# Performance work log

Measured on AMD Instinct MI355X. Metric: run time of the kernel, lower is better.

The kernel has to match this reference:

```python
import jax, jax.numpy as jnp
import numpy as np

B_, J_, D_, E_, N_, K_ = 32, 1024, 192, 384, 16, 3


def _dwconv(x, w, b):
    # x: (B,J,E), w: (E,1,K) depthwise, b: (E,)
    xc = jnp.transpose(x, (0, 2, 1))  # (B,E,J)
    pad = w.shape[2] // 2
    y = jax.lax.conv_general_dilated(
        xc, w, window_strides=(1,), padding=[(pad, pad)],
        feature_group_count=w.shape[0], dimension_numbers=('NCH', 'OIH', 'NCH'))
    return jnp.transpose(y + b[None, :, None], (0, 2, 1))  # (B,J,E)


def _scan_dir(x, cw, cb, WB, bB, WC, bC, WD, bD, A, Wi, bi, Wr, br):
    # One directional selective-SSM pass. x: (B,J,E); A: (N,) negative diag.
    xc = _dwconv(x, cw, cb)                       # (B,J,E)
    Bt = xc @ WB + bB                             # (B,J,N)
    Ct = xc @ WC + bC                             # (B,J,N)
    Dt = jax.nn.softplus(xc @ WD + bD)            # Delta, (B,J,N)
    A_bar = jnp.exp(Dt * A)                       # ZOH discretization
    B_bar = (A_bar - 1.0) / (A + 1e-6) * Bt
    u = xc @ Wi + bi                              # in_to_state, (B,J,N)
    Bu = B_bar * u

    def step(h, ab_bu):
        ab, bu = ab_bu
        h = ab * h + bu
        return h, h

    h0 = jnp.zeros((x.shape[0], A.shape[0]), x.dtype)
    _, hs = jax.lax.scan(step, h0, (jnp.swapaxes(A_bar, 0, 1), jnp.swapaxes(Bu, 0, 1)))
    hs = jnp.swapaxes(hs, 0, 1)                   # (B,J,N)
    return (hs * Ct) @ Wr + br                    # readout, (B,J,E)


def setup_inputs() -> dict:
    key = jax.random.key(0)
    ks = iter(jax.random.split(key, 40))

    def nrm(shape, scale=0.02):
        return jax.random.normal(next(ks), shape, jnp.float32) * scale

    inp = {
        'tokens': jax.random.normal(next(ks), (B_, J_, D_), jnp.float32),
        'norm_g': jnp.ones((D_,), jnp.float32),
        'norm_b': jnp.zeros((D_,), jnp.float32),
        'Wx': nrm((D_, E_)), 'bx': jnp.zeros((E_,), jnp.float32),
        'Wz': nrm((D_, E_)), 'bz': jnp.zeros((E_,), jnp.float32),
        'convf_w': nrm((E_, 1, K_), 0.1), 'convf_b': jnp.zeros((E_,), jnp.float32),
        'convb_w': nrm((E_, 1, K_), 0.1), 'convb_b': jnp.zeros((E_,), jnp.float32),
        'WBf': nrm((E_, N_)), 'bBf': jnp.zeros((N_,), jnp.float32),
        'WCf': nrm((E_, N_)), 'bCf': jnp.zeros((N_,), jnp.float32),
        'WDf': nrm((E_, N_)), 'bDf': jnp.zeros((N_,), jnp.float32),
        'WBb': nrm((E_, N_)), 'bBb': jnp.zeros((N_,), jnp.float32),
        'WCb': nrm((E_, N_)), 'bCb': jnp.zeros((N_,), jnp.float32),
        'WDb': nrm((E_, N_)), 'bDb': jnp.zeros((N_,), jnp.float32),
        'A_log': nrm((N_,), 0.5),
        'Wi': nrm((E_, N_)), 'bi': jnp.zeros((N_,), jnp.float32),
        'Wr': nrm((N_, E_)), 'br': jnp.zeros((E_,), jnp.float32),
        'Wo': nrm((E_, D_)), 'bo': jnp.zeros((D_,), jnp.float32),
    }
    return inp


def reference(tokens, norm_g, norm_b, Wx, bx, Wz, bz, convf_w, convf_b,
              convb_w, convb_b, WBf, bBf, WCf, bCf, WDf, bDf, WBb, bBb,
              WCb, bCb, WDb, bDb, A_log, Wi, bi, Wr, br, Wo, bo):
    # LayerNorm (biased variance, eps=1e-5, like torch)
    mu = jnp.mean(tokens, axis=-1, keepdims=True)
    var = jnp.mean(jnp.square(tokens - mu), axis=-1, keepdims=True)
    t = (tokens - mu) / jnp.sqrt(var + 1e-5) * norm_g + norm_b

    x = t @ Wx + bx
    z = t @ Wz + bz
    gate = jax.nn.sigmoid(jax.nn.silu(z))

    # A computed under no_grad in torch -> stop_gradient here
    A = jax.lax.stop_gradient(-jax.nn.softplus(A_log))

    y_f = _scan_dir(x, convf_w, convf_b, WBf, bBf, WCf, bCf, WDf, bDf, A, Wi, bi, Wr, br)
    y_b = jnp.flip(_scan_dir(jnp.flip(x, 1), convb_w, convb_b, WBb, bBb, WCb, bCb,
                             WDb, bDb, A, Wi, bi, Wr, br), 1)
    y = (y_f + y_b) * gate
    return tokens + y @ Wo + bo
```

## Files before the change

### kernel.cpp

```cpp
#include <hip/hip_runtime.h>
#include <math.h>


typedef __attribute__((ext_vector_type(8))) short short8;
typedef __attribute__((ext_vector_type(4))) float f32x4;

__device__ __forceinline__ unsigned short f2bf(float f){
  union { float f; unsigned u; } v; v.f = f;
  unsigned r = v.u + 0x7FFFu + ((v.u >> 16) & 1u);
  return (unsigned short)(r >> 16);
}
__device__ __forceinline__ float bf2f(unsigned short s){
  union { unsigned u; float f; } v; v.u = ((unsigned)s) << 16;
  return v.f;
}
__device__ __forceinline__ float softplusf(float x){
  return (x > 20.f) ? x : log1pf(expf(x));
}
__device__ __forceinline__ float softplus_fast(float x){
  return (x > 20.f) ? x : __logf(1.f + __expf(x));
}
__device__ __forceinline__ float sigf_fast(float x){
  return __builtin_amdgcn_rcpf(1.f + __expf(-x));
}

__global__ __launch_bounds__(256) void prep_kernel(
    const float* __restrict__ Wx, const float* __restrict__ Wz,
    const float* __restrict__ WBf, const float* __restrict__ WCf,
    const float* __restrict__ WDf, const float* __restrict__ WBb,
    const float* __restrict__ WCb, const float* __restrict__ WDb,
    const float* __restrict__ Wi, const float* __restrict__ Wr,
    const float* __restrict__ Wo,
    const float* __restrict__ bBf, const float* __restrict__ bCf,
    const float* __restrict__ bDf, const float* __restrict__ bBb,
    const float* __restrict__ bCb, const float* __restrict__ bDb,
    const float* __restrict__ bi,
    unsigned short* __restrict__ Wxz_t, unsigned short* __restrict__ W4f_t,
    unsigned short* __restrict__ W4b_t, unsigned short* __restrict__ Wrt2,
    unsigned short* __restrict__ Wot, float* __restrict__ b4f,
    float* __restrict__ b4b)
{
  int idx = blockIdx.x * 256 + threadIdx.x;
  if (idx < 147456){ int n = idx / 192, k = idx % 192;
    Wxz_t[idx] = f2bf(n < 384 ? Wx[k*384 + n] : Wz[k*384 + n - 384]); return; }
  idx -= 147456;
  if (idx < 24576){ int n = idx / 384, k = idx % 384;
    const float* W = (n<16)?WBf:(n<32)?WCf:(n<48)?WDf:Wi;
    W4f_t[idx] = f2bf(W[k*16 + (n&15)]); return; }
  idx -= 24576;
  if (idx < 24576){ int n = idx / 384, k = idx % 384;
    const float* W = (n<16)?WBb:(n<32)?WCb:(n<48)?WDb:Wi;
    W4b_t[idx] = f2bf(W[k*16 + (n&15)]); return; }
  idx -= 24576;
  if (idx < 12288){ int n = idx / 32, k = idx % 32;
    Wrt2[idx] = f2bf(Wr[(k&15)*384 + n]); return; }
  idx -= 12288;
  if (idx < 73728){ int n = idx / 384, k = idx % 384;
    Wot[idx] = f2bf(Wo[k*192 + n]); return; }
  idx -= 73728;
  if (idx < 64){
    const float* bsel = (idx<16)?bBf:(idx<32)?bCf:(idx<48)?bDf:bi;
    b4f[idx] = bsel[idx & 15]; return; }
  idx -= 64;
  if (idx < 64){
    const float* bsel = (idx<16)?bBb:(idx<32)?bCb:(idx<48)?bDb:bi;
    b4b[idx] = bsel[idx & 15]; return; }
}

__global__ __launch_bounds__(256) void ln_kernel(
    const float* __restrict__ tokens, const float* __restrict__ g,
    const float* __restrict__ nb, unsigned short* __restrict__ t_bf)
{
  __shared__ unsigned short s[32 * 200];
  const int t = threadIdx.x;
  const int row0 = blockIdx.x * 32;
  {
    const int r = t >> 3, l8 = t & 7;
    const float* tr = tokens + (long)(row0 + r) * 192;
    float v[24], sm = 0.f, sq = 0.f;
#pragma unroll
    for (int i = 0; i < 24; i++){ float x = tr[l8 + 8*i]; v[i] = x; sm += x; sq += x*x; }
#pragma unroll
    for (int m = 1; m < 8; m <<= 1){ sm += __shfl_xor(sm, m); sq += __shfl_xor(sq, m); }
    const float mu = sm * (1.f/192.f);
    const float rstd = rsqrtf(sq * (1.f/192.f) - mu*mu + 1e-5f);
#pragma unroll
    for (int i = 0; i < 24; i++){
      const int d = l8 + 8*i;
      s[r*200 + d] = f2bf((v[i] - mu)*rstd*g[d] + nb[d]);
    }
  }
  __syncthreads();
  {
#pragma unroll
    for (int i = 0; i < 3; i++){
      const int item = i*256 + t;
      const int row = item / 24, c8 = item % 24;
      *(short8*)&t_bf[(long)(row0 + row)*192 + c8*8] =
          *(const short8*)&s[row*200 + c8*8];
    }
  }
}

__global__ __launch_bounds__(256) void xz_gemm(
    const unsigned short* __restrict__ t_bf,
    const unsigned short* __restrict__ Wxz_t,
    const float* __restrict__ bx, const float* __restrict__ bz,
    unsigned short* __restrict__ x_bf, unsigned short* __restrict__ gate_bf)
{
  __shared__ unsigned short tl[64 * 200];
  const int t = threadIdx.x;
  const int ct = blockIdx.x % 6;
  const int rt = blockIdx.x / 6;
  const int row0 = rt * 64;

  {
#pragma unroll
    for (int i = 0; i < 6; i++){
      const int item = i*256 + t;
      const int row = item / 24, c8 = item % 24;
      *(short8*)&tl[row*200 + c8*8] =
          *(const short8*)&t_bf[(long)(row0 + row)*192 + c8*8];
    }
  }
  __syncthreads();

  const int lane = t & 63, w = t >> 6;
  const int l15 = lane & 15, q = lane >> 4;
  const int C0 = ct*128 + w*32;

  f32x4 acc[4][2];
#pragma unroll
  for (int m = 0; m < 4; m++)
#pragma unroll
    for (int nf = 0; nf < 2; nf++) acc[m][nf] = (f32x4){0.f,0.f,0.f,0.f};

  const unsigned short* wb = Wxz_t + (long)(C0 + l15)*192 + q*8;
#pragma unroll
  for (int ks = 0; ks < 6; ks++){
    const int k0 = ks * 32;
    short8 a0 = *(const short8*)&tl[(     l15)*200 + k0 + q*8];
    short8 a1 = *(const short8*)&tl[(16 + l15)*200 + k0 + q*8];
    short8 a2 = *(const short8*)&tl[(32 + l15)*200 + k0 + q*8];
    short8 a3 = *(const short8*)&tl[(48 + l15)*200 + k0 + q*8];
#pragma unroll
    for (int nf = 0; nf < 2; nf++){
      short8 bw = *(const short8*)&wb[nf*16*192 + k0];
      acc[0][nf] = __builtin_amdgcn_mfma_f32_16x16x32_bf16(a0, bw, acc[0][nf], 0, 0, 0);
      acc[1][nf] = __builtin_amdgcn_mfma_f32_16x16x32_bf16(a1, bw, acc[1][nf], 0, 0, 0);
      acc[2][nf] = __builtin_amdgcn_mfma_f32_16x16x32_bf16(a2, bw, acc[2][nf], 0, 0, 0);
      acc[3][nf] = __builtin_amdgcn_mfma_f32_16x16x32_bf16(a3, bw, acc[3][nf], 0, 0, 0);
    }
  }
  __syncthreads();

  unsigned short* stg = tl;
  const int isgate = (ct >= 3);
#pragma unroll
  for (int nf = 0; nf < 2; nf++){
    const int c = C0 + nf*16 + l15;
    const float bv = isgate ? bz[c - 384] : bx[c];
#pragma unroll
    for (int m = 0; m < 4; m++){
#pragma unroll
      for (int r = 0; r < 4; r++){
        float val = acc[m][nf][r] + bv;
        if (isgate){ const float si = val * sigf_fast(val); val = sigf_fast(si); }
        stg[(m*16 + q*4 + r)*136 + (w*32 + nf*16 + l15)] = f2bf(val);
      }
    }
  }
  __syncthreads();

  {
    unsigned short* outp = isgate ? gate_bf : x_bf;
    const int cb = isgate ? (ct*128 - 384) : (ct*128);
#pragma unroll
    for (int i = 0; i < 4; i++){
      const int item = i*256 + t;
      const int row = item / 16, c8 = item % 16;
      *(short8*)&outp[(long)(row0 + row)*384 + cb + c8*8] =
          *(const short8*)&stg[row*136 + c8*8];
    }
  }
}

__global__ __launch_bounds__(256) void proj_mfma(
    const unsigned short* __restrict__ x_bf,
    const float* __restrict__ cwf, const float* __restrict__ cbf,
    const float* __restrict__ cwb, const float* __restrict__ cbb,
    const unsigned short* __restrict__ W4f, const unsigned short* __restrict__ W4b,
    const float* __restrict__ b4f, const float* __restrict__ b4b,
    const float* __restrict__ A_log,
    float* __restrict__ Af, float* __restrict__ Buf, float* __restrict__ Ctf,
    float* __restrict__ Ab, float* __restrict__ Bub, float* __restrict__ Ctb)
{
  __shared__ unsigned short xc[32 * 392];
  float* pj = (float*)xc;
  const int t = threadIdx.x;
  const int dir = blockIdx.x >> 10;
  const int bid = blockIdx.x & 1023;
  const int b  = bid >> 5;
  const int j0 = (bid & 31) * 32;
  const float* cw = dir ? cwb : cwf;
  const float* cb = dir ? cbb : cbf;
  const unsigned short* W4 = dir ? W4b : W4f;
  const float* b4 = dir ? b4b : b4f;
  float* Aout = dir ? Ab  : Af;
  float* Bout = dir ? Bub : Buf;
  float* Cout = dir ? Ctb : Ctf;

  {
    const long xrow = (long)b * 1024 * 384;
#pragma unroll
    for (int i = 0; i < 6; i++){
      const int idx = i*256 + t;
      const int r = idx / 48;
      const int e0 = (idx - r*48) * 8;
      const int jp = j0 + r;
      short8 xm = (short8){0,0,0,0,0,0,0,0};
      short8 xp = (short8){0,0,0,0,0,0,0,0};
      if (jp >= 1){
        const int js = dir ? 1024 - jp : jp - 1;
        xm = *(const short8*)&x_bf[xrow + (long)js*384 + e0];
      }
      short8 x0;
      {
        const int js = dir ? 1023 - jp : jp;
        x0 = *(const short8*)&x_bf[xrow + (long)js*384 + e0];
      }
      if (jp <= 1022){
        const int js = dir ? 1022 - jp : jp + 1;
        xp = *(const short8*)&x_bf[xrow + (long)js*384 + e0];
      }
      float wv[24], cbv[8];
#pragma unroll
      for (int v = 0; v < 6; v++)
        *(float4*)&wv[v*4] = *(const float4*)&cw[e0*3 + v*4];
#pragma unroll
      for (int v = 0; v < 2; v++)
        *(float4*)&cbv[v*4] = *(const float4*)&cb[e0 + v*4];
      short8 o;
#pragma unroll
      for (int m = 0; m < 8; m++){
        const float acc = fmaf(wv[3*m],   bf2f((unsigned short)xm[m]),
                          fmaf(wv[3*m+1], bf2f((unsigned short)x0[m]),
                          fmaf(wv[3*m+2], bf2f((unsigned short)xp[m]), cbv[m])));
        o[m] = (short)f2bf(acc);
      }
      *(short8*)&xc[r*392 + e0] = o;
    }
  }
  __syncthreads();

  const int lane = t & 63, w = t >> 6;
  const int l15 = lane & 15, q = lane >> 4;
  const int rt = w & 1, ng = w >> 1;
  f32x4 acc[2];
#pragma unroll
  for (int nf = 0; nf < 2; nf++) acc[nf] = (f32x4){0.f,0.f,0.f,0.f};
  const unsigned short* wb = W4 + (long)(ng*32 + l15)*384 + q*8;
#pragma unroll
  for (int ks = 0; ks < 12; ks++){
    const int k0 = ks * 32;
    short8 a = *(const short8*)&xc[(rt*16 + l15)*392 + k0 + q*8];
#pragma unroll
    for (int nf = 0; nf < 2; nf++){
      short8 bw = *(const short8*)&wb[nf*16*384 + k0];
      acc[nf] = __builtin_amdgcn_mfma_f32_16x16x32_bf16(a, bw, acc[nf], 0, 0, 0);
    }
  }
  __syncthreads();

  {
#pragma unroll
    for (int nf = 0; nf < 2; nf++){
      const int col = ng*32 + nf*16 + l15;
#pragma unroll
      for (int r = 0; r < 4; r++)
        pj[col*34 + rt*16 + q*4 + r] = acc[nf][r];
    }
  }
  __syncthreads();

  {
#pragma unroll
    for (int i = 0; i < 2; i++){
      const int idx = i*256 + t;
      const int n = idx >> 5, j = idx & 31;
      const float Bt  = pj[(     n)*34 + j] + b4[n];
      const float Ctv = pj[(16 + n)*34 + j] + b4[16 + n];
      const float dt  = softplus_fast(pj[(32 + n)*34 + j] + b4[32 + n]);
      const float u   = pj[(48 + n)*34 + j] + b4[48 + n];
      const float Av  = -softplusf(A_log[n]);
      const float ab  = __expf(dt * Av);
      const float bu  = (ab - 1.f) * __builtin_amdgcn_rcpf(Av + 1e-6f) * Bt * u;
      const int jp = j0 + j;
      const long base = ((long)b*16 + n) * 1024;
      Aout[base + jp] = ab;
      Bout[base + jp] = bu;
      Cout[base + (dir ? 1023 - jp : jp)] = Ctv;
    }
  }
}

__global__ __launch_bounds__(256) void scan2_kernel(
    const float* __restrict__ Af, const float* __restrict__ Buf, float* __restrict__ hsf,
    const float* __restrict__ Ab, const float* __restrict__ Bub, float* __restrict__ hsb)
{
  __shared__ float sA[256], sB[256];
  const int sel = blockIdx.x >> 9;
  const long base = (long)(blockIdx.x & 511) * 1024;
  const float* Abar = sel ? Ab  : Af;
  const float* Bu   = sel ? Bub : Buf;
  float* hs         = sel ? hsb : hsf;
  const int t = threadIdx.x;
  const float4 a4 = *reinterpret_cast<const float4*>(&Abar[base + t*4]);
  const float4 b4 = *reinterpret_cast<const float4*>(&Bu[base + t*4]);
  float A = a4.x, Bc = b4.x;
  Bc = fmaf(a4.y, Bc, b4.y); A *= a4.y;
  Bc = fmaf(a4.z, Bc, b4.z); A *= a4.z;
  Bc = fmaf(a4.w, Bc, b4.w); A *= a4.w;
  sA[t] = A; sB[t] = Bc;
  __syncthreads();
  for (int off = 1; off < 256; off <<= 1){
    const float cA = sA[t], cB = sB[t];
    float pA = 1.f, pB = 0.f;
    if (t >= off){ pA = sA[t - off]; pB = sB[t - off]; }
    __syncthreads();
    sA[t] = pA * cA;
    sB[t] = fmaf(cA, pB, cB);
    __syncthreads();
  }
  float h = (t > 0) ? sB[t - 1] : 0.f;
  float4 o;
  h = fmaf(a4.x, h, b4.x); o.x = h;
  h = fmaf(a4.y, h, b4.y); o.y = h;
  h = fmaf(a4.z, h, b4.z); o.z = h;
  h = fmaf(a4.w, h, b4.w); o.w = h;
  *reinterpret_cast<float4*>(&hs[base + t*4]) = o;
}

__global__ __launch_bounds__(256) void final_mfma(
    const float* __restrict__ tokens, const unsigned short* __restrict__ gate_bf,
    const float* __restrict__ hsf, const float* __restrict__ Ctf,
    const float* __restrict__ hsb, const float* __restrict__ Ctb,
    const unsigned short* __restrict__ Wrt2, const float* __restrict__ br,
    const unsigned short* __restrict__ Wot, const float* __restrict__ bo,
    float* __restrict__ out)
{
  __shared__ unsigned short s2[16 * 36];
  __shared__ float stgf[16 * 200];
  unsigned short* yg = (unsigned short*)stgf;
  const int t = threadIdx.x;
  const int b  = blockIdx.x >> 6;
  const int j0 = (blockIdx.x & 63) * 16;

  {
#pragma unroll
    for (int i = 0; i < 2; i++){
      const int idx = i*256 + t;
      const int j = idx & 15, kk = idx >> 4;
      float val;
      if (kk < 16){
        const long p = ((long)b*16 + kk)*1024 + j0 + j;
        val = hsf[p] * Ctf[p];
      } else {
        const long basen = ((long)b*16 + (kk - 16)) * 1024;
        val = hsb[basen + 1023 - (j0 + j)] * Ctb[basen + j0 + j];
      }
      s2[j*36 + kk] = f2bf(val);
    }
  }
  __syncthreads();

  const int lane = t & 63, w = t >> 6;
  const int l15 = lane & 15, q = lane >> 4;

  {
    short8 a = *(const short8*)&s2[l15*36 + q*8];
    const unsigned short* wbp = Wrt2 + (long)l15*32 + q*8;
#pragma unroll
    for (int i = 0; i < 6; i++){
      const int nf = w*6 + i;
      short8 bw = *(const short8*)&wbp[nf*16*32];
      f32x4 acc = (f32x4){0.f,0.f,0.f,0.f};
      acc = __builtin_amdgcn_mfma_f32_16x16x32_bf16(a, bw, acc, 0, 0, 0);
      const int c = nf*16 + l15;
      const float brv = 2.f * br[c];
#pragma unroll
      for (int r = 0; r < 4; r++)
        yg[(q*4 + r)*388 + c] = f2bf(acc[r] + brv);
    }
  }
  __syncthreads();

  {
#pragma unroll
    for (int i = 0; i < 3; i++){
      const int item = i*256 + t;
      const int row = item / 48;
      const int cb  = (item % 48) * 8;
      short8 y8 = *(const short8*)&yg[row*388 + cb];
      short8 g8 = *(const short8*)&gate_bf[((long)b*1024 + j0 + row)*384 + cb];
      short8 o;
#pragma unroll
      for (int m = 0; m < 8; m++)
        o[m] = (short)f2bf(bf2f((unsigned short)y8[m]) * bf2f((unsigned short)g8[m]));
      *(short8*)&yg[row*388 + cb] = o;
    }
  }
  __syncthreads();

  f32x4 acc[3];
  {
#pragma unroll
    for (int i = 0; i < 3; i++) acc[i] = (f32x4){0.f,0.f,0.f,0.f};
    const unsigned short* wbp = Wot + (long)l15*384 + q*8;
#pragma unroll
    for (int ks = 0; ks < 12; ks++){
      const int k0 = ks * 32;
      short8 a = *(const short8*)&yg[l15*388 + k0 + q*8];
#pragma unroll
      for (int i = 0; i < 3; i++){
        const int nf = w*3 + i;
        short8 bw = *(const short8*)&wbp[(long)nf*16*384 + k0];
        acc[i] = __builtin_amdgcn_mfma_f32_16x16x32_bf16(a, bw, acc[i], 0, 0, 0);
      }
    }
  }
  __syncthreads();

  {
    const int gq = q ^ (q >> 1);
#pragma unroll
    for (int i = 0; i < 3; i++){
      const int nf = w*3 + i;
      const int c = nf*16 + l15;
      const float bv = bo[c];
      const int scol = ((nf + gq) % 12)*16 + l15;
#pragma unroll
      for (int r = 0; r < 4; r++)
        stgf[(q*4 + r)*200 + scol] = acc[i][r] + bv;
    }
  }
  __syncthreads();

  {
#pragma unroll
    for (int i = 0; i < 3; i++){
      const int item = i*256 + t;
      const int row = item / 48;
      const int c4  = (item % 48) * 4;
      const int qq = (row >> 2) & 3;
      const int gg = qq ^ (qq >> 1);
      const int nf = c4 / 16;
      const int scol = ((nf + gg) % 12)*16 + (c4 % 16);
      float4 v = *(const float4*)&stgf[row*200 + scol];
      const long R = (long)b*1024 + j0 + row;
      const float4 tk = *(const float4*)&tokens[R*192 + c4];
      v.x += tk.x; v.y += tk.y; v.z += tk.z; v.w += tk.w;
      *(float4*)&out[R*192 + c4] = v;
    }
  }
}

extern "C" void kernel_launch(void* const* d_in, const int* in_sizes, int n_in,
                              void* d_out, int out_size, void* d_ws, size_t ws_size,
                              hipStream_t stream)
{
  const float* tokens  = (const float*)d_in[0];
  const float* norm_g  = (const float*)d_in[1];
  const float* norm_b  = (const float*)d_in[2];
  const float* Wx      = (const float*)d_in[3];
  const float* bx      = (const float*)d_in[4];
  const float* Wz      = (const float*)d_in[5];
  const float* bz      = (const float*)d_in[6];
  const float* convf_w = (const float*)d_in[7];
  const float* convf_b = (const float*)d_in[8];
  const float* convb_w = (const float*)d_in[9];
  const float* convb_b = (const float*)d_in[10];
  const float* WBf     = (const float*)d_in[11];
  const float* bBf     = (const float*)d_in[12];
  const float* WCf     = (const float*)d_in[13];
  const float* bCf     = (const float*)d_in[14];
  const float* WDf     = (const float*)d_in[15];
  const float* bDf     = (const float*)d_in[16];
  const float* WBb     = (const float*)d_in[17];
  const float* bBb     = (const float*)d_in[18];
  const float* WCb     = (const float*)d_in[19];
  const float* bCb     = (const float*)d_in[20];
  const float* WDb     = (const float*)d_in[21];
  const float* bDb     = (const float*)d_in[22];
  const float* A_log   = (const float*)d_in[23];
  const float* Wi      = (const float*)d_in[24];
  const float* bi      = (const float*)d_in[25];
  const float* Wr      = (const float*)d_in[26];
  const float* br      = (const float*)d_in[27];
  const float* Wo      = (const float*)d_in[28];
  const float* bo      = (const float*)d_in[29];

  char* ws = (char*)d_ws;
  unsigned short* x_bf    = (unsigned short*)(ws + 0);
  unsigned short* gate_bf = (unsigned short*)(ws + 25165824);
  unsigned short* Wxz_t   = (unsigned short*)(ws + 50331648);
  unsigned short* W4f_t   = (unsigned short*)(ws + 50626560);
  unsigned short* W4b_t   = (unsigned short*)(ws + 50675712);
  unsigned short* Wrt2    = (unsigned short*)(ws + 50724864);
  unsigned short* Wot     = (unsigned short*)(ws + 50749440);
  float* b4f = (float*)(ws + 50896896);
  float* b4b = (float*)(ws + 50897152);
  float* Af  = (float*)(ws + 50897408);
  float* Buf = (float*)(ws + 52994560);
  float* Ctf = (float*)(ws + 55091712);
  float* hsf = (float*)(ws + 57188864);
  float* Ab  = (float*)(ws + 59286016);
  float* Bub = (float*)(ws + 61383168);
  float* Ctb = (float*)(ws + 63480320);
  float* hsb = (float*)(ws + 65577472);
  unsigned short* t_bf = (unsigned short*)(ws + 67674624);

  prep_kernel<<<1105, 256, 0, stream>>>(Wx, Wz, WBf, WCf, WDf, WBb, WCb, WDb,
                                        Wi, Wr, Wo, bBf, bCf, bDf, bBb, bCb, bDb, bi,
                                        Wxz_t, W4f_t, W4b_t, Wrt2, Wot, b4f, b4b);
  ln_kernel<<<1024, 256, 0, stream>>>(tokens, norm_g, norm_b, t_bf);
  xz_gemm<<<3072, 256, 0, stream>>>(t_bf, Wxz_t, bx, bz, x_bf, gate_bf);
  proj_mfma<<<2048, 256, 0, stream>>>(x_bf, convf_w, convf_b, convb_w, convb_b,
                                      W4f_t, W4b_t, b4f, b4b, A_log,
                                      Af, Buf, Ctf, Ab, Bub, Ctb);
  scan2_kernel<<<1024, 256, 0, stream>>>(Af, Buf, hsf, Ab, Bub, hsb);
  final_mfma<<<2048, 256, 0, stream>>>(tokens, gate_bf, hsf, Ctf, hsb, Ctb,
                                       Wrt2, br, Wot, bo, (float*)d_out);
}
```

Before: 139.1 us.

## Give each wave its own 16-row tile in final kernel and drop block syncs

The final readout/output kernel now assigns one 16-row tile to each wavefront instead of one per block. Each wave builds its own MFMA A-operand from hs*Ct, computes all 24 readout column tiles, and fuses the gate multiply into the output GEMM's operand load. Output is written straight from accumulators, removing every __syncthreads and the LDS staging for the store. In exchange each wave does four times more MFMA work and holds more accumulator registers. The final stores and the uncoalesced hs/Ct gathers may reduce memory efficiency.

```diff
diff --git a/kernel.cpp b/kernel.cpp
--- a/kernel.cpp
+++ b/kernel.cpp
@@ -349,118 +349,81 @@
     const unsigned short* __restrict__ Wot, const float* __restrict__ bo,
     float* __restrict__ out)
 {
-  __shared__ unsigned short s2[16 * 36];
-  __shared__ float stgf[16 * 200];
-  unsigned short* yg = (unsigned short*)stgf;
+  __shared__ unsigned short yg_all[4][16 * 392];
   const int t = threadIdx.x;
-  const int b  = blockIdx.x >> 6;
-  const int j0 = (blockIdx.x & 63) * 16;
-
-  {
-#pragma unroll
-    for (int i = 0; i < 2; i++){
-      const int idx = i*256 + t;
-      const int j = idx & 15, kk = idx >> 4;
-      float val;
-      if (kk < 16){
-        const long p = ((long)b*16 + kk)*1024 + j0 + j;
-        val = hsf[p] * Ctf[p];
-      } else {
-        const long basen = ((long)b*16 + (kk - 16)) * 1024;
-        val = hsb[basen + 1023 - (j0 + j)] * Ctb[basen + j0 + j];
-      }
-      s2[j*36 + kk] = f2bf(val);
-    }
-  }
-  __syncthreads();
-
-  const int lane = t & 63, w = t >> 6;
+  const int w = t >> 6, lane = t & 63;
   const int l15 = lane & 15, q = lane >> 4;
-
-  {
-    short8 a = *(const short8*)&s2[l15*36 + q*8];
+  const int gw = blockIdx.x * 4 + w;
+  const int b  = gw >> 6;
+  const int j0 = (gw & 63) * 16;
+  unsigned short* yg = &yg_all[w][0];
+
+  short8 a1;
+  {
+    const int row = j0 + l15;
+    if (q < 2){
+      const int kk0 = q * 8;
+#pragma unroll
+      for (int j = 0; j < 8; j++){
+        const long p = ((long)b*16 + kk0 + j)*1024 + row;
+        a1[j] = (short)f2bf(hsf[p] * Ctf[p]);
+      }
+    } else {
+      const int n0 = q * 8 - 16;
+#pragma unroll
+      for (int j = 0; j < 8; j++){
+        const long basen = ((long)b*16 + n0 + j) * 1024;
+        a1[j] = (short)f2bf(hsb[basen + 1023 - row] * Ctb[basen + row]);
+      }
+    }
+  }
+
+  {
     const unsigned short* wbp = Wrt2 + (long)l15*32 + q*8;
 #pragma unroll
-    for (int i = 0; i < 6; i++){
-      const int nf = w*6 + i;
+    for (int nf = 0; nf < 24; nf++){
       short8 bw = *(const short8*)&wbp[nf*16*32];
       f32x4 acc = (f32x4){0.f,0.f,0.f,0.f};
-      acc = __builtin_amdgcn_mfma_f32_16x16x32_bf16(a, bw, acc, 0, 0, 0);
+      acc = __builtin_amdgcn_mfma_f32_16x16x32_bf16(a1, bw, acc, 0, 0, 0);
       const int c = nf*16 + l15;
       const float brv = 2.f * br[c];
 #pragma unroll
       for (int r = 0; r < 4; r++)
-        yg[(q*4 + r)*388 + c] = f2bf(acc[r] + brv);
-    }
-  }
-  __syncthreads();
-
-  {
-#pragma unroll
-    for (int i = 0; i < 3; i++){
-      const int item = i*256 + t;
-      const int row = item / 48;
-      const int cb  = (item % 48) * 8;
-      short8 y8 = *(const short8*)&yg[row*388 + cb];
-      short8 g8 = *(const short8*)&gate_bf[((long)b*1024 + j0 + row)*384 + cb];
-      short8 o;
-#pragma unroll
-      for (int m = 0; m < 8; m++)
-        o[m] = (short)f2bf(bf2f((unsigned short)y8[m]) * bf2f((unsigned short)g8[m]));
-      *(short8*)&yg[row*388 + cb] = o;
-    }
-  }
-  __syncthreads();
-
-  f32x4 acc[3];
-  {
-#pragma unroll
-    for (int i = 0; i < 3; i++) acc[i] = (f32x4){0.f,0.f,0.f,0.f};
+        yg[(q*4 + r)*392 + c] = f2bf(acc[r] + brv);
+    }
+  }
+
+  f32x4 acc2[12];
+#pragma unroll
+  for (int i = 0; i < 12; i++) acc2[i] = (f32x4){0.f,0.f,0.f,0.f};
+  {
     const unsigned short* wbp = Wot + (long)l15*384 + q*8;
+    const long grow = ((long)b*1024 + j0 + l15) * 384;
 #pragma unroll
     for (int ks = 0; ks < 12; ks++){
       const int k0 = ks * 32;
-      short8 a = *(const short8*)&yg[l15*388 + k0 + q*8];
-#pragma unroll
-      for (int i = 0; i < 3; i++){
-        const int nf = w*3 + i;
-        short8 bw = *(const short8*)&wbp[(long)nf*16*384 + k0];
-        acc[i] = __builtin_amdgcn_mfma_f32_16x16x32_bf16(a, bw, acc[i], 0, 0, 0);
-      }
-    }
-  }
-  __syncthreads();
-
-  {
-    const int gq = q ^ (q >> 1);
-#pragma unroll
-    for (int i = 0; i < 3; i++){
-      const int nf = w*3 + i;
-      const int c = nf*16 + l15;
-      const float bv = bo[c];
-      const int scol = ((nf + gq) % 12)*16 + l15;
-#pragma unroll
-      for (int r = 0; r < 4; r++)
-        stgf[(q*4 + r)*200 + scol] = acc[i][r] + bv;
-    }
-  }
-  __syncthreads();
-
-  {
-#pragma unroll
-    for (int i = 0; i < 3; i++){
-      const int item = i*256 + t;
-      const int row = item / 48;
-      const int c4  = (item % 48) * 4;
-      const int qq = (row >> 2) & 3;
-      const int gg = qq ^ (qq >> 1);
-      const int nf = c4 / 16;
-      const int scol = ((nf + gg) % 12)*16 + (c4 % 16);
-      float4 v = *(const float4*)&stgf[row*200 + scol];
-      const long R = (long)b*1024 + j0 + row;
-      const float4 tk = *(const float4*)&tokens[R*192 + c4];
-      v.x += tk.x; v.y += tk.y; v.z += tk.z; v.w += tk.w;
-      *(float4*)&out[R*192 + c4] = v;
+      short8 y8 = *(const short8*)&yg[l15*392 + k0 + q*8];
+      short8 g8 = *(const short8*)&gate_bf[grow + k0 + q*8];
+      short8 a2;
+#pragma unroll
+      for (int m = 0; m < 8; m++)
+        a2[m] = (short)f2bf(bf2f((unsigned short)y8[m]) * bf2f((unsigned short)g8[m]));
+#pragma unroll
+      for (int i = 0; i < 12; i++){
+        short8 bw = *(const short8*)&wbp[(long)i*16*384 + k0];
+        acc2[i] = __builtin_amdgcn_mfma_f32_16x16x32_bf16(a2, bw, acc2[i], 0, 0, 0);
+      }
+    }
+  }
+
+#pragma unroll
+  for (int i = 0; i < 12; i++){
+    const int c = i*16 + l15;
+    const float bv = bo[c];
+#pragma unroll
+    for (int r = 0; r < 4; r++){
+      const long R = (long)b*1024 + j0 + q*4 + r;
+      out[R*192 + c] = tokens[R*192 + c] + acc2[i][r] + bv;
     }
   }
 }
@@ -529,6 +492,6 @@
                                       W4f_t, W4b_t, b4f, b4b, A_log,
                                       Af, Buf, Ctf, Ab, Bub, Ctb);
   scan2_kernel<<<1024, 256, 0, stream>>>(Af, Buf, hsf, Ab, Bub, hsb);
-  final_mfma<<<2048, 256, 0, stream>>>(tokens, gate_bf, hsf, Ctf, hsb, Ctb,
-                                       Wrt2, br, Wot, bo, (float*)d_out);
-}
+  final_mfma<<<512, 256, 0, stream>>>(tokens, gate_bf, hsf, Ctf, hsb, Ctb,
+                                      Wrt2, br, Wot, bo, (float*)d_out);
+}
```

Result: slower. 142.6 us (+2.5%).
